# Kernel tuning notes

Hardware: AMD Instinct MI355X
Metric: run time of the kernel (lower is better)

The kernel has to match this reference:

```python
import jax, jax.numpy as jnp
import numpy as np
from jax import lax

DIM = 128
HEADS = 4
B, H, W = 8, 128, 128


def conv1x1(x, w, b):
    # x: [B,C,H,W], w: [O,I,1,1]
    y = lax.conv_general_dilated(x, w, (1, 1), 'VALID',
                                 dimension_numbers=('NCHW', 'OIHW', 'NCHW'))
    return y + b[None, :, None, None]


def dwconv3x3(x, w, b):
    # depthwise: w: [C,1,3,3], groups=C
    C = x.shape[1]
    y = lax.conv_general_dilated(x, w, (1, 1), ((1, 1), (1, 1)),
                                 dimension_numbers=('NCHW', 'OIHW', 'NCHW'),
                                 feature_group_count=C)
    return y + b[None, :, None, None]


def setup_inputs() -> dict:
    key = jax.random.key(0)
    ks = jax.random.split(key, 7)
    s = 0.02
    return {
        'x': jax.random.normal(ks[0], (B, DIM, H, W), jnp.float32),
        'qkv_w': jax.random.normal(ks[1], (3 * DIM, DIM, 1, 1), jnp.float32) * s,
        'qkv_b': jnp.zeros((3 * DIM,), jnp.float32),
        'dw_w': jax.random.normal(ks[2], (3 * DIM, 1, 3, 3), jnp.float32) * s,
        'dw_b': jnp.zeros((3 * DIM,), jnp.float32),
        'proj_w': jax.random.normal(ks[3], (DIM, DIM, 1, 1), jnp.float32) * s,
        'proj_b': jnp.zeros((DIM,), jnp.float32),
        'temperature': jnp.ones((HEADS, 1, 1, 1), jnp.float32),
    }


def reference(x, qkv_w, qkv_b, dw_w, dw_b, proj_w, proj_b, temperature):
    b, C, h, w = x.shape
    heads = temperature.shape[0]
    c = C // heads

    qkv = dwconv3x3(conv1x1(x, qkv_w, qkv_b), dw_w, dw_b)
    q, k, v = jnp.split(qkv, 3, axis=1)

    # b (head c) h w -> b head c h w
    q = q.reshape(b, heads, c, h, w)
    k = k.reshape(b, heads, c, h, w)
    v = v.reshape(b, heads, c, h, w)

    # L2-normalize along H (axis=-2), matching torch F.normalize eps=1e-12
    eps = 1e-12
    q = q / jnp.maximum(jnp.linalg.norm(q, axis=-2, keepdims=True), eps)
    k = k / jnp.maximum(jnp.linalg.norm(k, axis=-2, keepdims=True), eps)

    # attn[b,n,c,j,k] = sum_i q[b,n,c,i,j] * k_[b,n,c,i,k]  -> [b,head,c,W,W]
    attn = jnp.einsum('bncij,bncik->bncjk', q, k) * temperature
    attn = jax.nn.softmax(attn, axis=-2)

    # out[b,n,c,i,k] = sum_j v[b,n,c,i,j] * attn[b,n,c,j,k]
    out = jnp.einsum('bncij,bncjk->bncik', v, attn)
    out = out.reshape(b, C, h, w)
    return conv1x1(out, proj_w, proj_b)
```

## Files before the change

### kernel.cpp

```cpp
#include <hip/hip_runtime.h>

typedef unsigned short u16;
typedef unsigned int   u32;

typedef short bf16x8 __attribute__((ext_vector_type(8)));
typedef float f32x4  __attribute__((ext_vector_type(4)));

__device__ __forceinline__ float bf2f(u16 u) { return __uint_as_float(((u32)u) << 16); }
__device__ __forceinline__ u16 f2bf(float f) {
    u32 u = __float_as_uint(f);
    return (u16)((u + 0x7fffu + ((u >> 16) & 1u)) >> 16);
}

#define MFMA16(a, b, c) __builtin_amdgcn_mfma_f32_16x16x32_bf16(a, b, c, 0, 0, 0)

__global__ __launch_bounds__(256, 4) void k_xpose(const float* __restrict__ x,
                                                  u16* __restrict__ xT) {
    __shared__ u16 Xs[128 * 128];
    const int ptile = blockIdx.x, b = blockIdx.y;
    const int t = threadIdx.x;
    const float* xb = x + (((size_t)b) << 21) + ptile * 128;
#pragma unroll
    for (int i = 0; i < 16; ++i) {
        int idx = i * 256 + t;
        int ci = idx >> 5, pq = idx & 31;
        float4 v = *(const float4*)(xb + (((size_t)ci) << 14) + pq * 4);
        u32 lo = (u32)f2bf(v.x) | ((u32)f2bf(v.y) << 16);
        u32 hi = (u32)f2bf(v.z) | ((u32)f2bf(v.w) << 16);
        uint2 pk; pk.x = lo; pk.y = hi;
        int cq = ci >> 3;
        *(uint2*)(&Xs[ci * 128 + ((pq ^ cq) << 2)]) = pk;
    }
    __syncthreads();
    u16* ob = xT + (((size_t)b) << 21) + ((size_t)(ptile * 128)) * 128;
#pragma unroll
    for (int j = 0; j < 8; ++j) {
        int p = j * 16 + (t >> 4), cq = t & 15;
        u16 tmp[8];
#pragma unroll
        for (int c = 0; c < 8; ++c) {
            int ci = cq * 8 + c;
            tmp[c] = Xs[ci * 128 + (((p >> 2) ^ cq) << 2) + (p & 3)];
        }
        *(uint4*)(&ob[(size_t)p * 128 + cq * 8]) = *(const uint4*)tmp;
    }
}

template <bool CM>
__global__ __launch_bounds__(512, 6) void k_qkv_t(const u16* __restrict__ xT,
                                                  const float* __restrict__ w,
                                                  const float* __restrict__ bias,
                                                  u16* __restrict__ out1,
                                                  int cgbase) {
    extern __shared__ char smem[];
    u16* Bt = (u16*)smem;
    u16* Cs = Bt + 2048 * 8;
    const int h = blockIdx.x, cg = blockIdx.y + cgbase, b = blockIdx.z;
    const int t = threadIdx.x;

    const u16* xb = xT + (((size_t)b) << 21) + (CM ? (h << 7) : (h << 14));
#pragma unroll
    for (int i = 0; i < 4; ++i) {
        int slot = i * 512 + t;
        int p = slot >> 4, g = slot & 15;
        int gg = g ^ (p & 15);
        uint4 v = *(const uint4*)(&xb[(CM ? (p << 14) : (p << 7)) + gg * 8]);
        *(uint4*)(&Bt[slot * 8]) = v;
    }

    const int wave = t >> 6, lane = t & 63, m16 = lane & 15, quad = lane >> 4;
    bf16x8 afr[4];
    {
        const float* wp0 = w + (size_t)(cg * 128 + wave * 16 + m16) * 128 + quad * 8;
#pragma unroll
        for (int kk = 0; kk < 4; ++kk) {
            float4 w0 = *(const float4*)(wp0 + kk * 32);
            float4 w1 = *(const float4*)(wp0 + kk * 32 + 4);
            bf16x8 a;
            a[0] = (short)f2bf(w0.x); a[1] = (short)f2bf(w0.y);
            a[2] = (short)f2bf(w0.z); a[3] = (short)f2bf(w0.w);
            a[4] = (short)f2bf(w1.x); a[5] = (short)f2bf(w1.y);
            a[6] = (short)f2bf(w1.z); a[7] = (short)f2bf(w1.w);
            afr[kk] = a;
        }
    }
    __syncthreads();

    f32x4 acc[8] = {};
#pragma unroll
    for (int kk = 0; kk < 4; ++kk) {
        const int g = kk * 4 + quad;
#pragma unroll
        for (int nt = 0; nt < 8; ++nt) {
            int p = nt * 16 + m16;
            bf16x8 bf = *(const bf16x8*)(&Bt[p * 128 + ((g ^ (p & 15)) << 3)]);
            acc[nt] = MFMA16(afr[kk], bf, acc[nt]);
        }
    }

    float bv[4];
#pragma unroll
    for (int r = 0; r < 4; ++r) bv[r] = bias[cg * 128 + wave * 16 + quad * 4 + r];

    u16* ob = out1 + (((size_t)(b * 384 + cg * 128)) << 14) + (h << 7);

    if (wave < 4) {
#pragma unroll
        for (int nt = 0; nt < 8; ++nt) {
            int p = nt * 16 + m16;
#pragma unroll
            for (int r = 0; r < 4; ++r)
                Cs[(wave * 16 + quad * 4 + r) * 136 + p] = f2bf(acc[nt][r] + bv[r]);
        }
    }
    __syncthreads();
#pragma unroll
    for (int it = 0; it < 2; ++it) {
        int idx = it * 512 + t;
        int co = idx >> 4, cp = idx & 15;
        *(uint4*)(&ob[((size_t)co << 14) + cp * 8]) = *(const uint4*)(&Cs[co * 136 + cp * 8]);
    }
    __syncthreads();

    if (wave >= 4) {
#pragma unroll
        for (int nt = 0; nt < 8; ++nt) {
            int p = nt * 16 + m16;
#pragma unroll
            for (int r = 0; r < 4; ++r)
                Cs[((wave - 4) * 16 + quad * 4 + r) * 136 + p] = f2bf(acc[nt][r] + bv[r]);
        }
    }
    __syncthreads();
    u16* ob2 = ob + ((size_t)64 << 14);
#pragma unroll
    for (int it = 0; it < 2; ++it) {
        int idx = it * 512 + t;
        int co = idx >> 4, cp = idx & 15;
        *(uint4*)(&ob2[((size_t)co << 14) + cp * 8]) = *(const uint4*)(&Cs[co * 136 + cp * 8]);
    }
}

__global__ __launch_bounds__(512, 4) void k_attn(const u16* __restrict__ qkv,
                                                 const float* __restrict__ dww,
                                                 const float* __restrict__ dwb,
                                                 const float* __restrict__ temp,
                                                 u16* __restrict__ outp) {
    extern __shared__ char smem[];
    u16* Qt = (u16*)smem;
    u16* Kt = Qt + 16384;
    u16* Vr = (u16*)smem;
    u16* Sg = Qt + 32768;
    float* rqk = (float*)(smem + 75328);
    u16* Pt = Qt;
    u16* Osh = Kt;

    const int ch = blockIdx.x, b = blockIdx.y;
    const int head = ch >> 5;
    const int t = threadIdx.x;
    const size_t qoff = ((size_t)(b * 384 + ch)) << 14;
    const size_t koff = qoff + ((size_t)128 << 14);
    const size_t voff = qoff + ((size_t)256 << 14);

    const int wave = t >> 6, lane = t & 63, m16 = lane & 15, quad = lane >> 4;

#pragma unroll
    for (int i = 0; i < 4; ++i) {
        int idx = i * 512 + t;
        int r = idx >> 4, c16 = idx & 15;
        *(uint4*)(&Vr[r * 144 + 8 + c16 * 8]) =
            *(const uint4*)(&qkv[voff + ((size_t)r << 7) + c16 * 8]);
    }
    if (t < 256) {
        int r = t >> 1, side = t & 1;
        uint4 z = {0, 0, 0, 0};
        *(uint4*)(&Vr[r * 144 + side * 136]) = z;
    }
    __syncthreads();

    bf16x8 vfr[4];
    {
        float wv9[9];
        const float* wp = dww + (size_t)(256 + ch) * 9;
#pragma unroll
        for (int i = 0; i < 9; ++i) wv9[i] = wp[i];
        const float bvv = dwb[256 + ch];
        const int r = wave * 16 + m16;
#pragma unroll
        for (int kk = 0; kk < 4; ++kk) {
            const int c0 = quad * 8 + kk * 32;
            float acc[8];
#pragma unroll
            for (int c = 0; c < 8; ++c) acc[c] = bvv;
#pragma unroll
            for (int dy = 0; dy < 3; ++dy) {
                int rr = r + dy - 1;
                if ((unsigned)rr < 128u) {
                    const u16* row = &Vr[rr * 144 + 8 + c0];
                    float v0 = bf2f(row[-1]);
                    uint4 m = *(const uint4*)row;
                    float v1 = bf2f((u16)(m.x & 0xffff)), v2 = bf2f((u16)(m.x >> 16));
                    float v3 = bf2f((u16)(m.y & 0xffff)), v4 = bf2f((u16)(m.y >> 16));
                    float v5 = bf2f((u16)(m.z & 0xffff)), v6 = bf2f((u16)(m.z >> 16));
                    float v7 = bf2f((u16)(m.w & 0xffff)), v8 = bf2f((u16)(m.w >> 16));
                    float v9 = bf2f(row[8]);
                    const float w0 = wv9[dy * 3], w1 = wv9[dy * 3 + 1], w2 = wv9[dy * 3 + 2];
                    acc[0] += w0 * v0 + w1 * v1 + w2 * v2;
                    acc[1] += w0 * v1 + w1 * v2 + w2 * v3;
                    acc[2] += w0 * v2 + w1 * v3 + w2 * v4;
                    acc[3] += w0 * v3 + w1 * v4 + w2 * v5;
                    acc[4] += w0 * v4 + w1 * v5 + w2 * v6;
                    acc[5] += w0 * v5 + w1 * v6 + w2 * v7;
                    acc[6] += w0 * v6 + w1 * v7 + w2 * v8;
                    acc[7] += w0 * v7 + w1 * v8 + w2 * v9;
                }
            }
            bf16x8 a;
#pragma unroll
            for (int c = 0; c < 8; ++c) a[c] = (short)f2bf(acc[c]);
            vfr[kk] = a;
        }
    }
    __syncthreads();

    if (t < 68) {
        int r = t >> 1, side = t & 1;
        uint4 z = {0, 0, 0, 0};
        *(uint4*)(&Sg[r * 144 + side * 136]) = z;
    }

    const int sr = t >> 4, sc16 = t & 15;
    const int jloc = t >> 4, seg = t & 15;

    {
        int grow = sr - 1;
        uint4 v = {0, 0, 0, 0};
        if ((unsigned)grow < 128u)
            v = *(const uint4*)(&qkv[qoff + ((size_t)grow << 7) + sc16 * 8]);
        *(uint4*)(&Sg[sr * 144 + 8 + sc16 * 8]) = v;
        if (t < 32) {
            int r2 = 32 + (t >> 4);
            int g2 = r2 - 1;
            uint4 v2 = {0, 0, 0, 0};
            if ((unsigned)g2 < 128u)
                v2 = *(const uint4*)(&qkv[qoff + ((size_t)g2 << 7) + sc16 * 8]);
            *(uint4*)(&Sg[r2 * 144 + 8 + sc16 * 8]) = v2;
        }
    }
    __syncthreads();

#pragma unroll 1
    for (int ph = 0; ph < 8; ++ph) {
        const int mat = ph >> 2;
        const int j0 = (ph & 3) * 32;
        const size_t moff = mat ? koff : qoff;

        uint4 pf0 = {0, 0, 0, 0}, pf1 = {0, 0, 0, 0};
        if (ph < 7) {
            const int matn = (ph + 1) >> 2;
            const int j0n = ((ph + 1) & 3) * 32;
            const size_t moffn = matn ? koff : qoff;
            int grow = j0n - 1 + sr;
            if ((unsigned)grow < 128u)
                pf0 = *(const uint4*)(&qkv[moffn + ((size_t)grow << 7) + sc16 * 8]);
            if (t < 32) {
                int g2 = j0n - 1 + 32 + (t >> 4);
                if ((unsigned)g2 < 128u)
                    pf1 = *(const uint4*)(&qkv[moffn + ((size_t)g2 << 7) + sc16 * 8]);
            }
        }
        (void)moff;

        float wg9[9];
        {
            const float* wp = dww + (size_t)(mat * 128 + ch) * 9;
#pragma unroll
            for (int i = 0; i < 9; ++i) wg9[i] = wp[i];
        }
        const float gb = dwb[mat * 128 + ch];

        float acc[8];
#pragma unroll
        for (int c = 0; c < 8; ++c) acc[c] = gb;
#pragma unroll
        for (int pr = 0; pr < 3; ++pr) {
            const u16* row = &Sg[(jloc + pr) * 144 + 8 + seg * 8];
            float v0 = bf2f(row[-1]);
            uint4 m = *(const uint4*)row;
            float v1 = bf2f((u16)(m.x & 0xffff)), v2 = bf2f((u16)(m.x >> 16));
            float v3 = bf2f((u16)(m.y & 0xffff)), v4 = bf2f((u16)(m.y >> 16));
            float v5 = bf2f((u16)(m.z & 0xffff)), v6 = bf2f((u16)(m.z >> 16));
            float v7 = bf2f((u16)(m.w & 0xffff)), v8 = bf2f((u16)(m.w >> 16));
            float v9 = bf2f(row[8]);
            const float w0 = wg9[pr], w1 = wg9[3 + pr], w2 = wg9[6 + pr];
            acc[0] += w0 * v0 + w1 * v1 + w2 * v2;
            acc[1] += w0 * v1 + w1 * v2 + w2 * v3;
            acc[2] += w0 * v2 + w1 * v3 + w2 * v4;
            acc[3] += w0 * v3 + w1 * v4 + w2 * v5;
            acc[4] += w0 * v4 + w1 * v5 + w2 * v6;
            acc[5] += w0 * v5 + w1 * v6 + w2 * v7;
            acc[6] += w0 * v6 + w1 * v7 + w2 * v8;
            acc[7] += w0 * v7 + w1 * v8 + w2 * v9;
        }
        u16 tmp[8];
        float ssq = 0.f;
#pragma unroll
        for (int c = 0; c < 8; ++c) {
            u16 uv = f2bf(acc[c]);
            tmp[c] = uv;
            float f = bf2f(uv);
            ssq += f * f;
        }
        ssq += __shfl_xor(ssq, 1);
        ssq += __shfl_xor(ssq, 2);
        ssq += __shfl_xor(ssq, 4);
        ssq += __shfl_xor(ssq, 8);
        const int j = j0 + jloc;
        if (seg == 0) rqk[mat * 128 + j] = ssq;
        u16* dst = (mat ? Kt : Qt) + j * 128 + ((seg ^ (j & 15)) << 3);
        *(uint4*)dst = *(const uint4*)tmp;

        __syncthreads();
        if (ph < 7) {
            *(uint4*)(&Sg[sr * 144 + 8 + sc16 * 8]) = pf0;
            if (t < 32) *(uint4*)(&Sg[(32 + (t >> 4)) * 144 + 8 + sc16 * 8]) = pf1;
        }
        __syncthreads();
    }

    if (t < 256) rqk[t] = 1.0f / fmaxf(sqrtf(rqk[t]), 1e-12f);
    __syncthreads();

    f32x4 S[8] = {};
#pragma unroll
    for (int kk = 0; kk < 4; ++kk) {
        const int sw = ((kk * 4 + quad) ^ m16) << 3;
        bf16x8 bf = *(const bf16x8*)(&Kt[(wave * 16 + m16) * 128 + sw]);
#pragma unroll
        for (int jt = 0; jt < 8; ++jt) {
            bf16x8 af = *(const bf16x8*)(&Qt[(jt * 16 + m16) * 128 + sw]);
            S[jt] = MFMA16(af, bf, S[jt]);
        }
    }

    const float sc = temp[head] * rqk[128 + wave * 16 + m16];
    float vals[8][4];
    float vmax = -1e30f;
#pragma unroll
    for (int jt = 0; jt < 8; ++jt)
#pragma unroll
        for (int r = 0; r < 4; ++r) {
            float v = S[jt][r] * (rqk[jt * 16 + quad * 4 + r] * sc);
            vals[jt][r] = v;
            vmax = fmaxf(vmax, v);
        }
    vmax = fmaxf(vmax, __shfl_xor(vmax, 16));
    vmax = fmaxf(vmax, __shfl_xor(vmax, 32));
    float sum = 0.f;
#pragma unroll
    for (int jt = 0; jt < 8; ++jt)
#pragma unroll
        for (int r = 0; r < 4; ++r) {
            float e = __expf(vals[jt][r] - vmax);
            vals[jt][r] = e;
            sum += e;
        }
    sum += __shfl_xor(sum, 16);
    sum += __shfl_xor(sum, 32);
    const float inv = 1.0f / sum;

    __syncthreads();

    {
        const int k = wave * 16 + m16;
        u16* prow = Pt + k * 128;
#pragma unroll
        for (int jt = 0; jt < 8; ++jt)
#pragma unroll
            for (int pr = 0; pr < 2; ++pr) {
                int j0w = jt * 16 + quad * 4 + pr * 2;
                u32 pk = (u32)f2bf(vals[jt][pr * 2] * inv) |
                         ((u32)f2bf(vals[jt][pr * 2 + 1] * inv) << 16);
                *(u32*)(prow + (((j0w >> 3) ^ (k & 15)) << 3) + (j0w & 7)) = pk;
            }
    }
    __syncthreads();

    f32x4 O[8] = {};
#pragma unroll
    for (int kk = 0; kk < 4; ++kk) {
        const int sw = ((kk * 4 + quad) ^ m16) << 3;
#pragma unroll
        for (int nt = 0; nt < 8; ++nt) {
            bf16x8 bf = *(const bf16x8*)(&Pt[(nt * 16 + m16) * 128 + sw]);
            O[nt] = MFMA16(vfr[kk], bf, O[nt]);
        }
    }

#pragma unroll
    for (int nt = 0; nt < 8; ++nt) {
        int k = nt * 16 + m16;
#pragma unroll
        for (int r = 0; r < 4; ++r) {
            int i = wave * 16 + quad * 4 + r;
            Osh[i * 128 + (((k >> 3) ^ (i & 15)) << 3) + (k & 7)] = f2bf(O[nt][r]);
        }
    }
    __syncthreads();

    u16* ob = outp + (((size_t)(b * 128 + ch)) << 14);
#pragma unroll
    for (int it = 0; it < 4; ++it) {
        int idx = it * 512 + t;
        int row = idx >> 4, gk = idx & 15;
        uint4 v = *(const uint4*)(&Osh[row * 128 + ((gk ^ (row & 15)) << 3)]);
        *(uint4*)(&ob[(row << 7) + gk * 8]) = v;
    }
}

__global__ __launch_bounds__(512, 6) void k_proj(const u16* __restrict__ ain,
                                                 const float* __restrict__ w,
                                                 const float* __restrict__ bias,
                                                 float* __restrict__ outp) {
    extern __shared__ char smem[];
    u16* Bt = (u16*)smem;
    u16* Sg = Bt + 16384;
    const int h = blockIdx.x, b = blockIdx.y;
    const int t = threadIdx.x;

    const int ldr = t >> 4, ldj8 = t & 15;
    const int gig = t >> 7, gp = t & 127;
    const u16* gcol = &Sg[(gig * 8) * 144 + gp];
    u16* gdst = Bt + gp * 128;
#pragma unroll
    for (int ph = 0; ph < 4; ++ph) {
        int ch = ph * 32 + ldr;
        *(uint4*)(&Sg[ldr * 144 + ldj8 * 8]) =
            *(const uint4*)(&ain[(((size_t)(b * 128 + ch)) << 14) + (h << 7) + ldj8 * 8]);
        __syncthreads();
        u16 tmp[8];
#pragma unroll
        for (int c = 0; c < 8; ++c) tmp[c] = gcol[c * 144];
        int g = ph * 4 + gig;
        *(uint4*)(gdst + ((g ^ (gp & 15)) << 3)) = *(const uint4*)tmp;
        __syncthreads();
    }

    const int wave = t >> 6, lane = t & 63, m16 = lane & 15, quad = lane >> 4;
    bf16x8 afr[4];
    {
        const float* wp0 = w + (size_t)(wave * 16 + m16) * 128 + quad * 8;
#pragma unroll
        for (int kk = 0; kk < 4; ++kk) {
            float4 w0 = *(const float4*)(wp0 + kk * 32);
            float4 w1 = *(const float4*)(wp0 + kk * 32 + 4);
            bf16x8 a;
            a[0] = (short)f2bf(w0.x); a[1] = (short)f2bf(w0.y);
            a[2] = (short)f2bf(w0.z); a[3] = (short)f2bf(w0.w);
            a[4] = (short)f2bf(w1.x); a[5] = (short)f2bf(w1.y);
            a[6] = (short)f2bf(w1.z); a[7] = (short)f2bf(w1.w);
            afr[kk] = a;
        }
    }

    f32x4 acc[8] = {};
#pragma unroll
    for (int kk = 0; kk < 4; ++kk) {
        const int g = kk * 4 + quad;
#pragma unroll
        for (int nt = 0; nt < 8; ++nt) {
            int p = nt * 16 + m16;
            bf16x8 bf = *(const bf16x8*)(&Bt[p * 128 + ((g ^ (p & 15)) << 3)]);
            acc[nt] = MFMA16(afr[kk], bf, acc[nt]);
        }
    }

    float bv[4];
#pragma unroll
    for (int r = 0; r < 4; ++r) bv[r] = bias[wave * 16 + quad * 4 + r];
    float* ob = outp + (((size_t)(b * 128)) << 14) + (h << 7);
#pragma unroll
    for (int nt = 0; nt < 8; ++nt) {
        int p = nt * 16 + m16;
#pragma unroll
        for (int r = 0; r < 4; ++r) {
            int co = wave * 16 + quad * 4 + r;
            ob[((size_t)co << 14) + p] = acc[nt][r] + bv[r];
        }
    }
}

extern "C" void kernel_launch(void* const* d_in, const int* in_sizes, int n_in,
                              void* d_out, int out_size, void* d_ws, size_t ws_size,
                              hipStream_t stream) {
    const float* x      = (const float*)d_in[0];
    const float* qkv_w  = (const float*)d_in[1];
    const float* qkv_b  = (const float*)d_in[2];
    const float* dw_w   = (const float*)d_in[3];
    const float* dw_b   = (const float*)d_in[4];
    const float* proj_w = (const float*)d_in[5];
    const float* proj_b = (const float*)d_in[6];
    const float* temp   = (const float*)d_in[7];
    float* out = (float*)d_out;

    u16* buf1 = (u16*)d_ws;
    u16* buf2 = buf1 + (size_t)8 * 384 * 16384;

    hipFuncSetAttribute((const void*)k_qkv_t<true>,  hipFuncAttributeMaxDynamicSharedMemorySize, 50176);
    hipFuncSetAttribute((const void*)k_qkv_t<false>, hipFuncAttributeMaxDynamicSharedMemorySize, 50176);
    hipFuncSetAttribute((const void*)k_attn, hipFuncAttributeMaxDynamicSharedMemorySize, 76352);
    hipFuncSetAttribute((const void*)k_proj, hipFuncAttributeMaxDynamicSharedMemorySize, 41984);

    k_xpose<<<dim3(128, 8), 256, 0, stream>>>(x, buf2);
    k_qkv_t<true><<<dim3(128, 2, 8), 512, 50176, stream>>>(buf2, qkv_w, qkv_b, buf1, 0);
    k_qkv_t<false><<<dim3(128, 1, 8), 512, 50176, stream>>>(buf2, qkv_w, qkv_b, buf1, 2);
    k_attn<<<dim3(128, 8), 512, 76352, stream>>>(buf1, dw_w, dw_b, temp, buf2);
    k_proj<<<dim3(128, 8), 512, 41984, stream>>>(buf2, proj_w, proj_b, out);
}
```

Baseline: 248.0 us.

## Keep K fragments in registers and reuse one LDS region to halve attention shared memory

The attention kernel now loads V, then K, then Q in sequence into a single padded LDS region and runs each depthwise conv from there. K's conv output and its inverse norm stay in registers as MFMA B fragments instead of being written to a separate Kt buffer. The 8-phase prefetch pipeline goes away, and dynamic shared memory drops from about 76 KB to about 37 KB so that more blocks fit per CU (launch bounds raised to 6). The trade-off is serialized global loads with extra barriers, no overlap of loads with compute, and higher register pressure from holding kfr and the Q tiles.

```diff
diff --git a/kernel.cpp b/kernel.cpp
--- a/kernel.cpp
+++ b/kernel.cpp
@@ -141,19 +141,17 @@
     }
 }
 
-__global__ __launch_bounds__(512, 4) void k_attn(const u16* __restrict__ qkv,
+__global__ __launch_bounds__(512, 6) void k_attn(const u16* __restrict__ qkv,
                                                  const float* __restrict__ dww,
                                                  const float* __restrict__ dwb,
                                                  const float* __restrict__ temp,
                                                  u16* __restrict__ outp) {
     extern __shared__ char smem[];
+    u16* R0 = (u16*)smem;
     u16* Qt = (u16*)smem;
-    u16* Kt = Qt + 16384;
-    u16* Vr = (u16*)smem;
-    u16* Sg = Qt + 32768;
-    float* rqk = (float*)(smem + 75328);
+    float* rqk = (float*)(smem + 36864);
     u16* Pt = Qt;
-    u16* Osh = Kt;
+    u16* Osh = Qt;
 
     const int ch = blockIdx.x, b = blockIdx.y;
     const int head = ch >> 5;
@@ -163,40 +161,40 @@
     const size_t voff = qoff + ((size_t)256 << 14);
 
     const int wave = t >> 6, lane = t & 63, m16 = lane & 15, quad = lane >> 4;
+    const int wr = wave * 16 + m16;
 
 #pragma unroll
     for (int i = 0; i < 4; ++i) {
         int idx = i * 512 + t;
         int r = idx >> 4, c16 = idx & 15;
-        *(uint4*)(&Vr[r * 144 + 8 + c16 * 8]) =
+        *(uint4*)(&R0[r * 144 + 8 + c16 * 8]) =
             *(const uint4*)(&qkv[voff + ((size_t)r << 7) + c16 * 8]);
     }
     if (t < 256) {
         int r = t >> 1, side = t & 1;
         uint4 z = {0, 0, 0, 0};
-        *(uint4*)(&Vr[r * 144 + side * 136]) = z;
+        *(uint4*)(&R0[r * 144 + side * 136]) = z;
     }
     __syncthreads();
 
     bf16x8 vfr[4];
     {
-        float wv9[9];
+        float w9[9];
         const float* wp = dww + (size_t)(256 + ch) * 9;
 #pragma unroll
-        for (int i = 0; i < 9; ++i) wv9[i] = wp[i];
-        const float bvv = dwb[256 + ch];
-        const int r = wave * 16 + m16;
+        for (int i = 0; i < 9; ++i) w9[i] = wp[i];
+        const float gb = dwb[256 + ch];
 #pragma unroll
         for (int kk = 0; kk < 4; ++kk) {
             const int c0 = quad * 8 + kk * 32;
             float acc[8];
 #pragma unroll
-            for (int c = 0; c < 8; ++c) acc[c] = bvv;
+            for (int c = 0; c < 8; ++c) acc[c] = gb;
 #pragma unroll
             for (int dy = 0; dy < 3; ++dy) {
-                int rr = r + dy - 1;
+                int rr = wr + dy - 1;
                 if ((unsigned)rr < 128u) {
-                    const u16* row = &Vr[rr * 144 + 8 + c0];
+                    const u16* row = &R0[rr * 144 + 8 + c0];
                     float v0 = bf2f(row[-1]);
                     uint4 m = *(const uint4*)row;
                     float v1 = bf2f((u16)(m.x & 0xffff)), v2 = bf2f((u16)(m.x >> 16));
@@ -204,7 +202,7 @@
                     float v5 = bf2f((u16)(m.z & 0xffff)), v6 = bf2f((u16)(m.z >> 16));
                     float v7 = bf2f((u16)(m.w & 0xffff)), v8 = bf2f((u16)(m.w >> 16));
                     float v9 = bf2f(row[8]);
-                    const float w0 = wv9[dy * 3], w1 = wv9[dy * 3 + 1], w2 = wv9[dy * 3 + 2];
+                    const float w0 = w9[dy * 3], w1 = w9[dy * 3 + 1], w2 = w9[dy * 3 + 2];
                     acc[0] += w0 * v0 + w1 * v1 + w2 * v2;
                     acc[1] += w0 * v1 + w1 * v2 + w2 * v3;
                     acc[2] += w0 * v2 + w1 * v3 + w2 * v4;
@@ -223,127 +221,154 @@
     }
     __syncthreads();
 
-    if (t < 68) {
-        int r = t >> 1, side = t & 1;
-        uint4 z = {0, 0, 0, 0};
-        *(uint4*)(&Sg[r * 144 + side * 136]) = z;
-    }
-
-    const int sr = t >> 4, sc16 = t & 15;
-    const int jloc = t >> 4, seg = t & 15;
-
+#pragma unroll
+    for (int i = 0; i < 4; ++i) {
+        int idx = i * 512 + t;
+        int r = idx >> 4, c16 = idx & 15;
+        *(uint4*)(&R0[r * 144 + 8 + c16 * 8]) =
+            *(const uint4*)(&qkv[koff + ((size_t)r << 7) + c16 * 8]);
+    }
+    __syncthreads();
+
+    bf16x8 kfr[4];
+    float rkinv;
     {
-        int grow = sr - 1;
-        uint4 v = {0, 0, 0, 0};
-        if ((unsigned)grow < 128u)
-            v = *(const uint4*)(&qkv[qoff + ((size_t)grow << 7) + sc16 * 8]);
-        *(uint4*)(&Sg[sr * 144 + 8 + sc16 * 8]) = v;
-        if (t < 32) {
-            int r2 = 32 + (t >> 4);
-            int g2 = r2 - 1;
-            uint4 v2 = {0, 0, 0, 0};
-            if ((unsigned)g2 < 128u)
-                v2 = *(const uint4*)(&qkv[qoff + ((size_t)g2 << 7) + sc16 * 8]);
-            *(uint4*)(&Sg[r2 * 144 + 8 + sc16 * 8]) = v2;
-        }
-    }
-    __syncthreads();
-
-#pragma unroll 1
-    for (int ph = 0; ph < 8; ++ph) {
-        const int mat = ph >> 2;
-        const int j0 = (ph & 3) * 32;
-        const size_t moff = mat ? koff : qoff;
-
-        uint4 pf0 = {0, 0, 0, 0}, pf1 = {0, 0, 0, 0};
-        if (ph < 7) {
-            const int matn = (ph + 1) >> 2;
-            const int j0n = ((ph + 1) & 3) * 32;
-            const size_t moffn = matn ? koff : qoff;
-            int grow = j0n - 1 + sr;
-            if ((unsigned)grow < 128u)
-                pf0 = *(const uint4*)(&qkv[moffn + ((size_t)grow << 7) + sc16 * 8]);
-            if (t < 32) {
-                int g2 = j0n - 1 + 32 + (t >> 4);
-                if ((unsigned)g2 < 128u)
-                    pf1 = *(const uint4*)(&qkv[moffn + ((size_t)g2 << 7) + sc16 * 8]);
+        float w9[9];
+        const float* wp = dww + (size_t)(128 + ch) * 9;
+#pragma unroll
+        for (int i = 0; i < 9; ++i) w9[i] = wp[i];
+        const float gb = dwb[128 + ch];
+        float ssq = 0.f;
+#pragma unroll
+        for (int kk = 0; kk < 4; ++kk) {
+            const int c0 = quad * 8 + kk * 32;
+            float acc[8];
+#pragma unroll
+            for (int c = 0; c < 8; ++c) acc[c] = gb;
+#pragma unroll
+            for (int pr = 0; pr < 3; ++pr) {
+                int rr = wr + pr - 1;
+                if ((unsigned)rr < 128u) {
+                    const u16* row = &R0[rr * 144 + 8 + c0];
+                    float v0 = bf2f(row[-1]);
+                    uint4 m = *(const uint4*)row;
+                    float v1 = bf2f((u16)(m.x & 0xffff)), v2 = bf2f((u16)(m.x >> 16));
+                    float v3 = bf2f((u16)(m.y & 0xffff)), v4 = bf2f((u16)(m.y >> 16));
+                    float v5 = bf2f((u16)(m.z & 0xffff)), v6 = bf2f((u16)(m.z >> 16));
+                    float v7 = bf2f((u16)(m.w & 0xffff)), v8 = bf2f((u16)(m.w >> 16));
+                    float v9 = bf2f(row[8]);
+                    const float w0 = w9[pr], w1 = w9[3 + pr], w2 = w9[6 + pr];
+                    acc[0] += w0 * v0 + w1 * v1 + w2 * v2;
+                    acc[1] += w0 * v1 + w1 * v2 + w2 * v3;
+                    acc[2] += w0 * v2 + w1 * v3 + w2 * v4;
+                    acc[3] += w0 * v3 + w1 * v4 + w2 * v5;
+                    acc[4] += w0 * v4 + w1 * v5 + w2 * v6;
+                    acc[5] += w0 * v5 + w1 * v6 + w2 * v7;
+                    acc[6] += w0 * v6 + w1 * v7 + w2 * v8;
+                    acc[7] += w0 * v7 + w1 * v8 + w2 * v9;
+                }
             }
-        }
-        (void)moff;
-
-        float wg9[9];
-        {
-            const float* wp = dww + (size_t)(mat * 128 + ch) * 9;
-#pragma unroll
-            for (int i = 0; i < 9; ++i) wg9[i] = wp[i];
-        }
-        const float gb = dwb[mat * 128 + ch];
-
-        float acc[8];
-#pragma unroll
-        for (int c = 0; c < 8; ++c) acc[c] = gb;
-#pragma unroll
-        for (int pr = 0; pr < 3; ++pr) {
-            const u16* row = &Sg[(jloc + pr) * 144 + 8 + seg * 8];
-            float v0 = bf2f(row[-1]);
-            uint4 m = *(const uint4*)row;
-            float v1 = bf2f((u16)(m.x & 0xffff)), v2 = bf2f((u16)(m.x >> 16));
-            float v3 = bf2f((u16)(m.y & 0xffff)), v4 = bf2f((u16)(m.y >> 16));
-            float v5 = bf2f((u16)(m.z & 0xffff)), v6 = bf2f((u16)(m.z >> 16));
-            float v7 = bf2f((u16)(m.w & 0xffff)), v8 = bf2f((u16)(m.w >> 16));
-            float v9 = bf2f(row[8]);
-            const float w0 = wg9[pr], w1 = wg9[3 + pr], w2 = wg9[6 + pr];
-            acc[0] += w0 * v0 + w1 * v1 + w2 * v2;
-            acc[1] += w0 * v1 + w1 * v2 + w2 * v3;
-            acc[2] += w0 * v2 + w1 * v3 + w2 * v4;
-            acc[3] += w0 * v3 + w1 * v4 + w2 * v5;
-            acc[4] += w0 * v4 + w1 * v5 + w2 * v6;
-            acc[5] += w0 * v5 + w1 * v6 + w2 * v7;
-            acc[6] += w0 * v6 + w1 * v7 + w2 * v8;
-            acc[7] += w0 * v7 + w1 * v8 + w2 * v9;
-        }
-        u16 tmp[8];
-        float ssq = 0.f;
-#pragma unroll
-        for (int c = 0; c < 8; ++c) {
-            u16 uv = f2bf(acc[c]);
-            tmp[c] = uv;
-            float f = bf2f(uv);
-            ssq += f * f;
-        }
-        ssq += __shfl_xor(ssq, 1);
-        ssq += __shfl_xor(ssq, 2);
-        ssq += __shfl_xor(ssq, 4);
-        ssq += __shfl_xor(ssq, 8);
-        const int j = j0 + jloc;
-        if (seg == 0) rqk[mat * 128 + j] = ssq;
-        u16* dst = (mat ? Kt : Qt) + j * 128 + ((seg ^ (j & 15)) << 3);
-        *(uint4*)dst = *(const uint4*)tmp;
-
-        __syncthreads();
-        if (ph < 7) {
-            *(uint4*)(&Sg[sr * 144 + 8 + sc16 * 8]) = pf0;
-            if (t < 32) *(uint4*)(&Sg[(32 + (t >> 4)) * 144 + 8 + sc16 * 8]) = pf1;
-        }
-        __syncthreads();
-    }
-
-    if (t < 256) rqk[t] = 1.0f / fmaxf(sqrtf(rqk[t]), 1e-12f);
+            bf16x8 a;
+#pragma unroll
+            for (int c = 0; c < 8; ++c) {
+                u16 uv = f2bf(acc[c]);
+                a[c] = (short)uv;
+                float f = bf2f(uv);
+                ssq += f * f;
+            }
+            kfr[kk] = a;
+        }
+        ssq += __shfl_xor(ssq, 16);
+        ssq += __shfl_xor(ssq, 32);
+        rkinv = 1.0f / fmaxf(sqrtf(ssq), 1e-12f);
+    }
+    __syncthreads();
+
+#pragma unroll
+    for (int i = 0; i < 4; ++i) {
+        int idx = i * 512 + t;
+        int r = idx >> 4, c16 = idx & 15;
+        *(uint4*)(&R0[r * 144 + 8 + c16 * 8]) =
+            *(const uint4*)(&qkv[qoff + ((size_t)r << 7) + c16 * 8]);
+    }
+    __syncthreads();
+
+    const int jr0 = t >> 4, seg = t & 15;
+    uint4 qt4[4];
+    {
+        float w9[9];
+        const float* wp = dww + (size_t)ch * 9;
+#pragma unroll
+        for (int i = 0; i < 9; ++i) w9[i] = wp[i];
+        const float gb = dwb[ch];
+#pragma unroll
+        for (int pass = 0; pass < 4; ++pass) {
+            const int j = pass * 32 + jr0;
+            float acc[8];
+#pragma unroll
+            for (int c = 0; c < 8; ++c) acc[c] = gb;
+#pragma unroll
+            for (int pr = 0; pr < 3; ++pr) {
+                int rr = j + pr - 1;
+                if ((unsigned)rr < 128u) {
+                    const u16* row = &R0[rr * 144 + 8 + seg * 8];
+                    float v0 = bf2f(row[-1]);
+                    uint4 m = *(const uint4*)row;
+                    float v1 = bf2f((u16)(m.x & 0xffff)), v2 = bf2f((u16)(m.x >> 16));
+                    float v3 = bf2f((u16)(m.y & 0xffff)), v4 = bf2f((u16)(m.y >> 16));
+                    float v5 = bf2f((u16)(m.z & 0xffff)), v6 = bf2f((u16)(m.z >> 16));
+                    float v7 = bf2f((u16)(m.w & 0xffff)), v8 = bf2f((u16)(m.w >> 16));
+                    float v9 = bf2f(row[8]);
+                    const float w0 = w9[pr], w1 = w9[3 + pr], w2 = w9[6 + pr];
+                    acc[0] += w0 * v0 + w1 * v1 + w2 * v2;
+                    acc[1] += w0 * v1 + w1 * v2 + w2 * v3;
+                    acc[2] += w0 * v2 + w1 * v3 + w2 * v4;
+                    acc[3] += w0 * v3 + w1 * v4 + w2 * v5;
+                    acc[4] += w0 * v4 + w1 * v5 + w2 * v6;
+                    acc[5] += w0 * v5 + w1 * v6 + w2 * v7;
+                    acc[6] += w0 * v6 + w1 * v7 + w2 * v8;
+                    acc[7] += w0 * v7 + w1 * v8 + w2 * v9;
+                }
+            }
+            u16 tmp[8];
+            float ssq = 0.f;
+#pragma unroll
+            for (int c = 0; c < 8; ++c) {
+                u16 uv = f2bf(acc[c]);
+                tmp[c] = uv;
+                float f = bf2f(uv);
+                ssq += f * f;
+            }
+            ssq += __shfl_xor(ssq, 1);
+            ssq += __shfl_xor(ssq, 2);
+            ssq += __shfl_xor(ssq, 4);
+            ssq += __shfl_xor(ssq, 8);
+            if (seg == 0) rqk[j] = ssq;
+            qt4[pass] = *(const uint4*)tmp;
+        }
+    }
+    __syncthreads();
+
+#pragma unroll
+    for (int pass = 0; pass < 4; ++pass) {
+        const int j = pass * 32 + jr0;
+        *(uint4*)(&Qt[j * 128 + ((seg ^ (j & 15)) << 3)]) = qt4[pass];
+    }
+    if (t < 128) rqk[t] = 1.0f / fmaxf(sqrtf(rqk[t]), 1e-12f);
     __syncthreads();
 
     f32x4 S[8] = {};
 #pragma unroll
     for (int kk = 0; kk < 4; ++kk) {
         const int sw = ((kk * 4 + quad) ^ m16) << 3;
-        bf16x8 bf = *(const bf16x8*)(&Kt[(wave * 16 + m16) * 128 + sw]);
 #pragma unroll
         for (int jt = 0; jt < 8; ++jt) {
             bf16x8 af = *(const bf16x8*)(&Qt[(jt * 16 + m16) * 128 + sw]);
-            S[jt] = MFMA16(af, bf, S[jt]);
-        }
-    }
-
-    const float sc = temp[head] * rqk[128 + wave * 16 + m16];
+            S[jt] = MFMA16(af, kfr[kk], S[jt]);
+        }
+    }
+
+    const float sc = temp[head] * rkinv;
     float vals[8][4];
     float vmax = -1e30f;
 #pragma unroll
@@ -372,7 +397,7 @@
     __syncthreads();
 
     {
-        const int k = wave * 16 + m16;
+        const int k = wr;
         u16* prow = Pt + k * 128;
 #pragma unroll
         for (int jt = 0; jt < 8; ++jt)
@@ -396,6 +421,7 @@
             O[nt] = MFMA16(vfr[kk], bf, O[nt]);
         }
     }
+    __syncthreads();
 
 #pragma unroll
     for (int nt = 0; nt < 8; ++nt) {
@@ -508,12 +534,12 @@
 
     hipFuncSetAttribute((const void*)k_qkv_t<true>,  hipFuncAttributeMaxDynamicSharedMemorySize, 50176);
     hipFuncSetAttribute((const void*)k_qkv_t<false>, hipFuncAttributeMaxDynamicSharedMemorySize, 50176);
-    hipFuncSetAttribute((const void*)k_attn, hipFuncAttributeMaxDynamicSharedMemorySize, 76352);
+    hipFuncSetAttribute((const void*)k_attn, hipFuncAttributeMaxDynamicSharedMemorySize, 37376);
     hipFuncSetAttribute((const void*)k_proj, hipFuncAttributeMaxDynamicSharedMemorySize, 41984);
 
     k_xpose<<<dim3(128, 8), 256, 0, stream>>>(x, buf2);
     k_qkv_t<true><<<dim3(128, 2, 8), 512, 50176, stream>>>(buf2, qkv_w, qkv_b, buf1, 0);
     k_qkv_t<false><<<dim3(128, 1, 8), 512, 50176, stream>>>(buf2, qkv_w, qkv_b, buf1, 2);
-    k_attn<<<dim3(128, 8), 512, 76352, stream>>>(buf1, dw_w, dw_b, temp, buf2);
+    k_attn<<<dim3(128, 8), 512, 37376, stream>>>(buf1, dw_w, dw_b, temp, buf2);
     k_proj<<<dim3(128, 8), 512, 41984, stream>>>(buf2, proj_w, proj_b, out);
 }
```

Result: slower. 338.0 us (+36.3%).
